# Kernel optimization log

Hardware: AMD Instinct MI355X
Metric: run time of the kernel (lower is better)

The kernel has to match this reference:

```python
import jax, jax.numpy as jnp
import numpy as np

COMMITMENT_COST = 0.25
LAMBDA_KL = 1.0
EPS = 1e-10


def setup_inputs() -> dict:
    key = jax.random.key(0)
    k1, k2 = jax.random.split(key)
    x = jax.random.normal(k1, (8, 4096, 256), dtype=jnp.float32)
    embedding = jax.random.normal(k2, (1024, 256), dtype=jnp.float32)
    return {"x": x, "embedding": embedding}


def reference(x, embedding):
    B, T, D = x.shape
    M, _ = embedding.shape
    x_sg = jax.lax.stop_gradient(x)
    x_flat = x_sg.reshape(-1, D)  # [N, D]
    distances = (jnp.sum(embedding ** 2, axis=1)[None, :]
                 + jnp.sum(x_flat ** 2, axis=1, keepdims=True)
                 - 2.0 * (x_flat @ embedding.T))  # [N, M]
    indices = jnp.argmin(distances.astype(jnp.float32), axis=-1)  # [N]
    quantized = embedding[indices].reshape(B, T, D)
    # losses (x detached in both terms, matching torch)
    loss = (COMMITMENT_COST * jnp.mean((x_sg - quantized) ** 2)
            + jnp.mean((quantized - x_sg) ** 2)) * LAMBDA_KL
    # straight-through estimator
    quantized_st = x + jax.lax.stop_gradient(quantized - x)
    # avg of one-hot encodings == normalized code counts (avoids NxM one-hot)
    N = B * T
    counts = jnp.zeros((M,), dtype=jnp.float32).at[indices].add(1.0)
    avg_probs = counts / N
    perplexity = jnp.exp(-jnp.sum(avg_probs * jnp.log(avg_probs + EPS)))
    return (quantized_st, loss, indices.reshape(B, T), perplexity)
```

## Files before the change

### kernel.cpp

```cpp
#include <hip/hip_runtime.h>


constexpr int D = 256;
constexpr int M = 1024;
constexpr int ROWS = 64;

typedef _Float16 f16;
typedef __attribute__((ext_vector_type(8))) _Float16 f16x8;
typedef __attribute__((ext_vector_type(4))) float f32x4;

constexpr size_t WS_ENORM_F = 1028;
constexpr size_t WS_TAB_B   = 8320;
constexpr size_t WS_NEEDED  = 1056896;

__device__ inline void gload_lds16(const void* g, void* l) {
    __builtin_amdgcn_global_load_lds(
        (const __attribute__((address_space(1))) unsigned int*)(g),
        (__attribute__((address_space(3))) unsigned int*)(l), 16, 0, 0);
}

__global__ __launch_bounds__(256) void prep_kernel(const float* __restrict__ e,
                                                   float* __restrict__ ws) {
    const int b = blockIdx.x, t = threadIdx.x;
    if (b < 256) {
        int v    = b * 256 + t;
        int lane = v & 63, unit = v >> 6;
        int spl = unit & 1, kk = (unit >> 1) & 7, t16 = unit >> 4;
        int lr = lane & 15, q = lane >> 4;
        const float* p = e + (size_t)(t16 * 16 + lr) * D + kk * 32 + q * 8;
        f32x4 a = *reinterpret_cast<const f32x4*>(p);
        f32x4 c = *reinterpret_cast<const f32x4*>(p + 4);
        f16 h0=(f16)a.x,h1=(f16)a.y,h2=(f16)a.z,h3=(f16)a.w;
        f16 h4=(f16)c.x,h5=(f16)c.y,h6=(f16)c.z,h7=(f16)c.w;
        f16x8 out;
        if (spl == 0) out = (f16x8){h0,h1,h2,h3,h4,h5,h6,h7};
        else          out = (f16x8){(f16)(a.x-(float)h0),(f16)(a.y-(float)h1),
                                    (f16)(a.z-(float)h2),(f16)(a.w-(float)h3),
                                    (f16)(c.x-(float)h4),(f16)(c.y-(float)h5),
                                    (f16)(c.z-(float)h6),(f16)(c.w-(float)h7)};
        *reinterpret_cast<f16x8*>((char*)ws + WS_TAB_B + (size_t)v * 16) = out;
    } else {
        int row  = (b - 256) * 4 + (t >> 6);
        int lane = t & 63;
        f32x4 a = *reinterpret_cast<const f32x4*>(e + (size_t)row * D + lane * 4);
        float s = fmaf(a.x, a.x, fmaf(a.y, a.y, fmaf(a.z, a.z, a.w * a.w)));
#pragma unroll
        for (int o = 32; o > 0; o >>= 1) s += __shfl_down(s, o, 64);
        if (lane == 0) ws[WS_ENORM_F + row] = s;
    }
}

__global__ __launch_bounds__(256, 2) void vq_fused_kernel(
    const float* __restrict__ x, const float* __restrict__ e,
    float* __restrict__ outQ, float* __restrict__ outIdx, float* __restrict__ ws)
{
    __shared__ ushort ebuf[2][2][8192];
    __shared__ float  en_s[M];
    __shared__ float  wval[4][32];
    __shared__ int    widx[4][32];
    __shared__ float  xns[ROWS];
    __shared__ int    fidx[ROWS];

    const int tid   = threadIdx.x;
    const int w     = __builtin_amdgcn_readfirstlane(tid >> 6);
    const int l     = tid & 63;
    const int lr    = l & 15, q = l >> 4;
    const int rpair = w >> 1;
    const int mhalf = w & 1;
    const int R     = blockIdx.x * ROWS;
    const char* tab = (const char*)ws + WS_TAB_B;

    auto stage = [&](int buf, int g) {
#pragma unroll
        for (int i = 0; i < 8; ++i) {
            int S = w * 8 + i, half = S >> 4, sg = S & 15;
            gload_lds16(tab + (size_t)(g + half * 32) * 16384 + sg * 1024 + l * 16,
                        &ebuf[buf][half][sg * 512]);
        }
    };
    stage(0, 0);

    {
        f32x4 v = *reinterpret_cast<const f32x4*>(ws + WS_ENORM_F + tid * 4);
        *reinterpret_cast<f32x4*>(&en_s[tid * 4]) = v;
    }

    f16x8 Xh[2][8], Xl[2][8];
    float xn[2];
#pragma unroll
    for (int cf = 0; cf < 2; ++cf) {
        float s = 0.f;
#pragma unroll
        for (int kk = 0; kk < 8; ++kk) {
            const float* p = x + (size_t)(R + rpair * 32 + cf * 16 + lr) * D + kk * 32 + q * 8;
            f32x4 a = *reinterpret_cast<const f32x4*>(p);
            f32x4 c = *reinterpret_cast<const f32x4*>(p + 4);
            f16 h0=(f16)a.x,h1=(f16)a.y,h2=(f16)a.z,h3=(f16)a.w;
            f16 h4=(f16)c.x,h5=(f16)c.y,h6=(f16)c.z,h7=(f16)c.w;
            Xh[cf][kk] = (f16x8){h0,h1,h2,h3,h4,h5,h6,h7};
            Xl[cf][kk] = (f16x8){(f16)(a.x-(float)h0),(f16)(a.y-(float)h1),
                                 (f16)(a.z-(float)h2),(f16)(a.w-(float)h3),
                                 (f16)(c.x-(float)h4),(f16)(c.y-(float)h5),
                                 (f16)(c.z-(float)h6),(f16)(c.w-(float)h7)};
            s = fmaf(a.x,a.x,fmaf(a.y,a.y,fmaf(a.z,a.z,fmaf(a.w,a.w,
                fmaf(c.x,c.x,fmaf(c.y,c.y,fmaf(c.z,c.z,fmaf(c.w,c.w,s))))))));
        }
        s += __shfl_xor(s, 16, 64);
        s += __shfl_xor(s, 32, 64);
        xn[cf] = s;
    }
    __syncthreads();

    float bV[2] = {3.4e38f, 3.4e38f};
    int   bI[2] = {0, 0};

    for (int g = 0; g < 32; ++g) {
        const ushort* eb = &ebuf[g & 1][mhalf][0];
        if (g < 31) stage((g + 1) & 1, g + 1);

        f32x4 accA0 = (f32x4){0.f,0.f,0.f,0.f};
        f32x4 accB0 = (f32x4){0.f,0.f,0.f,0.f};
        f32x4 accA1 = (f32x4){0.f,0.f,0.f,0.f};
        f32x4 accB1 = (f32x4){0.f,0.f,0.f,0.f};
        __builtin_amdgcn_s_setprio(1);
#pragma unroll
        for (int kk = 0; kk < 8; ++kk) {
            f16x8 Ah = *reinterpret_cast<const f16x8*>(eb + (kk*2+0)*512 + l*8);
            f16x8 Al = *reinterpret_cast<const f16x8*>(eb + (kk*2+1)*512 + l*8);
            accA0 = __builtin_amdgcn_mfma_f32_16x16x32_f16(Ah, Xh[0][kk], accA0, 0, 0, 0);
            accA1 = __builtin_amdgcn_mfma_f32_16x16x32_f16(Ah, Xh[1][kk], accA1, 0, 0, 0);
            accB0 = __builtin_amdgcn_mfma_f32_16x16x32_f16(Al, Xh[0][kk], accB0, 0, 0, 0);
            accB1 = __builtin_amdgcn_mfma_f32_16x16x32_f16(Al, Xh[1][kk], accB1, 0, 0, 0);
            accA0 = __builtin_amdgcn_mfma_f32_16x16x32_f16(Ah, Xl[0][kk], accA0, 0, 0, 0);
            accA1 = __builtin_amdgcn_mfma_f32_16x16x32_f16(Ah, Xl[1][kk], accA1, 0, 0, 0);
        }
        __builtin_amdgcn_s_setprio(0);
        __syncthreads();

        const int mbase = mhalf * 512 + g * 16;
        f32x4 en4 = *reinterpret_cast<const f32x4*>(&en_s[mbase + q * 4]);
#pragma unroll
        for (int i = 0; i < 4; ++i) {
            int mi = mbase + q * 4 + i;
            float dv0 = fmaf(-2.f, accA0[i] + accB0[i], en4[i]);
            float dv1 = fmaf(-2.f, accA1[i] + accB1[i], en4[i]);
            if (dv0 < bV[0]) { bV[0] = dv0; bI[0] = mi; }
            if (dv1 < bV[1]) { bV[1] = dv1; bI[1] = mi; }
        }
    }

#pragma unroll
    for (int cf = 0; cf < 2; ++cf) {
#pragma unroll
        for (int mk = 16; mk <= 32; mk <<= 1) {
            float ov = __shfl_xor(bV[cf], mk, 64);
            int   oi = __shfl_xor(bI[cf], mk, 64);
            if (ov < bV[cf] || (ov == bV[cf] && oi < bI[cf])) { bV[cf] = ov; bI[cf] = oi; }
        }
    }
    if (q == 0) {
#pragma unroll
        for (int cf = 0; cf < 2; ++cf) {
            wval[w][cf * 16 + lr] = bV[cf];
            widx[w][cf * 16 + lr] = bI[cf];
        }
        if (mhalf == 0) {
#pragma unroll
            for (int cf = 0; cf < 2; ++cf)
                xns[rpair * 32 + cf * 16 + lr] = xn[cf];
        }
    }
    __syncthreads();

    if (tid < 64) {
        int r = tid, g2 = r >> 5, rr = r & 31;
        float v0 = wval[g2 * 2 + 0][rr]; int i0 = widx[g2 * 2 + 0][rr];
        float v1 = wval[g2 * 2 + 1][rr]; int i1 = widx[g2 * 2 + 1][rr];
        float fv; int fi;
        if (v1 < v0) { fv = v1; fi = i1; } else { fv = v0; fi = i0; }
        fidx[r] = fi;
        outIdx[R + r] = (float)fi;
        atomicAdd(ws + 1 + fi, 1.0f);
        float ls = fv + xns[r];
#pragma unroll
        for (int o = 32; o > 0; o >>= 1) ls += __shfl_down(ls, o, 64);
        if (r == 0) atomicAdd(ws, ls);
    }
    __syncthreads();

#pragma unroll
    for (int it = 0; it < 16; ++it) {
        int u = it * 256 + tid;
        int row = u >> 6, c4 = u & 63;
        f32x4 v = *reinterpret_cast<const f32x4*>(e + (size_t)fidx[row] * D + c4 * 4);
        __builtin_nontemporal_store(v, reinterpret_cast<f32x4*>(outQ + (size_t)(R + row) * D + c4 * 4));
    }
}

__global__ void enorm_kernel(const float* __restrict__ e, float* __restrict__ enorm) {
    int m = blockIdx.x, l = threadIdx.x;
    const f32x4 v = *reinterpret_cast<const f32x4*>(e + m * D + l * 4);
    float s = fmaf(v.x, v.x, fmaf(v.y, v.y, fmaf(v.z, v.z, v.w * v.w)));
#pragma unroll
    for (int o = 32; o > 0; o >>= 1) s += __shfl_down(s, o, 64);
    if (l == 0) enorm[m] = s;
}

__global__ __launch_bounds__(256, 2) void vq_main_kernel(
    const float* __restrict__ x, const float* __restrict__ e,
    float* __restrict__ outQ, float* __restrict__ outIdx, float* __restrict__ ws) {
    __shared__ f32x4 xs[64][64];
    __shared__ float cval[4][64];
    __shared__ int   cidx[4][64];
    __shared__ int   fidx[64];
    const int tid = threadIdx.x, row0 = blockIdx.x * 64;
#pragma unroll
    for (int it = 0; it < 16; ++it) {
        int f = it * 256 + tid, rr = f >> 6, c4 = f & 63;
        xs[rr][c4 ^ (rr & 7)] = *reinterpret_cast<const f32x4*>(x + (row0 + rr) * D + c4 * 4);
    }
    __syncthreads();
    const int r = tid & 63, c = __builtin_amdgcn_readfirstlane(tid >> 6), sw = r & 7;
    float xnorm = 0.f;
    if (c == 0) {
        f32x4 a = (f32x4){0.f,0.f,0.f,0.f};
        for (int d4 = 0; d4 < 64; ++d4) {
            f32x4 xv = xs[r][d4 ^ sw];
            a.x = fmaf(xv.x, xv.x, a.x); a.y = fmaf(xv.y, xv.y, a.y);
            a.z = fmaf(xv.z, xv.z, a.z); a.w = fmaf(xv.w, xv.w, a.w);
        }
        xnorm = (a.x + a.y) + (a.z + a.w);
    }
    const float* __restrict__ enorm = ws + WS_ENORM_F;
    float bestVal = 3.4e38f; int bestIdx = 0;
    for (int chunk = 0; chunk < M / 32; ++chunk) {
        const int m0 = chunk * 32 + c * 8;
        f32x4 acc[8];
#pragma unroll
        for (int mi = 0; mi < 8; ++mi) acc[mi] = (f32x4){0.f,0.f,0.f,0.f};
#pragma unroll 2
        for (int d4 = 0; d4 < 64; ++d4) {
            const f32x4 xv = xs[r][d4 ^ sw];
#pragma unroll
            for (int mi = 0; mi < 8; ++mi) {
                const f32x4 ev = *reinterpret_cast<const f32x4*>(e + (m0 + mi) * D + d4 * 4);
                acc[mi].x = fmaf(xv.x, ev.x, acc[mi].x); acc[mi].y = fmaf(xv.y, ev.y, acc[mi].y);
                acc[mi].z = fmaf(xv.z, ev.z, acc[mi].z); acc[mi].w = fmaf(xv.w, ev.w, acc[mi].w);
            }
        }
#pragma unroll
        for (int mi = 0; mi < 8; ++mi) {
            float dot = (acc[mi].x + acc[mi].y) + (acc[mi].z + acc[mi].w);
            float val = enorm[m0 + mi] - 2.0f * dot;
            if (val < bestVal) { bestVal = val; bestIdx = m0 + mi; }
        }
    }
    cval[c][r] = bestVal; cidx[c][r] = bestIdx;
    __syncthreads();
    if (c == 0) {
        float bv = bestVal; int bi = bestIdx;
#pragma unroll
        for (int cc = 1; cc < 4; ++cc) {
            float v = cval[cc][r]; int i = cidx[cc][r];
            if (v < bv || (v == bv && i < bi)) { bv = v; bi = i; }
        }
        fidx[r] = bi; outIdx[row0 + r] = (float)bi;
        atomicAdd(ws + 1 + bi, 1.0f);
        float dist = bv + xnorm;
#pragma unroll
        for (int o = 32; o > 0; o >>= 1) dist += __shfl_down(dist, o, 64);
        if (r == 0) atomicAdd(ws, dist);
    }
    __syncthreads();
#pragma unroll
    for (int it = 0; it < 16; ++it) {
        int f = it * 256 + tid, rr = f >> 6, c4 = f & 63;
        *reinterpret_cast<f32x4*>(outQ + (row0 + rr) * D + c4 * 4) =
            *reinterpret_cast<const f32x4*>(e + fidx[rr] * D + c4 * 4);
    }
}

__global__ void vq_final_kernel(const float* __restrict__ ws,
                                float* __restrict__ outLoss, float* __restrict__ outPpl,
                                float invN, float invND) {
    int t = threadIdx.x;
    float p = ws[1 + t] * invN;
    float term = p * logf(p + 1e-10f);
#pragma unroll
    for (int o = 32; o > 0; o >>= 1) term += __shfl_down(term, o, 64);
    __shared__ float s[16];
    if ((t & 63) == 0) s[t >> 6] = term;
    __syncthreads();
    if (t == 0) {
        float tot = 0.f;
#pragma unroll
        for (int i = 0; i < 16; ++i) tot += s[i];
        *outPpl  = expf(-tot);
        *outLoss = 1.25f * ws[0] * invND;
    }
}

extern "C" void kernel_launch(void* const* d_in, const int* in_sizes, int n_in,
                              void* d_out, int out_size, void* d_ws, size_t ws_size,
                              hipStream_t stream) {
    const float* x = (const float*)d_in[0];
    const float* e = (const float*)d_in[1];
    const int NX = in_sizes[0];
    const int N  = NX / D;

    float* out     = (float*)d_out;
    float* outQ    = out;
    float* outLoss = out + NX;
    float* outIdx  = out + NX + 1;
    float* outPpl  = out + NX + 1 + N;
    float* ws      = (float*)d_ws;

    (void)hipMemsetAsync(d_ws, 0, 4100, stream);
    if (ws_size >= WS_NEEDED && (N % ROWS) == 0) {
        prep_kernel<<<512, 256, 0, stream>>>(e, ws);
        vq_fused_kernel<<<N / ROWS, 256, 0, stream>>>(x, e, outQ, outIdx, ws);
    } else {
        enorm_kernel<<<M, 64, 0, stream>>>(e, ws + WS_ENORM_F);
        vq_main_kernel<<<N / 64, 256, 0, stream>>>(x, e, outQ, outIdx, ws);
    }
    vq_final_kernel<<<1, 1024, 0, stream>>>(ws, outLoss, outPpl,
                                            1.0f / (float)N, 1.0f / (float)NX);
}
```

Before: 86.48 us.

## Switch distance GEMM to 32x32x16 MFMA with re-laid-out codebook table

Replaces the 16x16x32 MFMA tiling with 32x32x16 MFMAs, so each wave handles 32 rows against 32 codes per tile and the k dimension is split across two staged buffers per tile. The prep kernel writes the f16 hi/lo codebook table in a matching layout, and the argmin epilogue is reworked for the new accumulator layout. The workspace memset is folded into an extra prep block to drop a separate memset launch. The larger MFMA shape is meant to raise matrix-core throughput and cut instruction count, at the cost of more VGPRs for X fragments and more syncs per tile.

```diff
diff --git a/kernel.cpp b/kernel.cpp
--- a/kernel.cpp
+++ b/kernel.cpp
@@ -6,8 +6,9 @@
 constexpr int ROWS = 64;
 
 typedef _Float16 f16;
-typedef __attribute__((ext_vector_type(8))) _Float16 f16x8;
-typedef __attribute__((ext_vector_type(4))) float f32x4;
+typedef __attribute__((ext_vector_type(8)))  _Float16 f16x8;
+typedef __attribute__((ext_vector_type(4)))  float f32x4;
+typedef __attribute__((ext_vector_type(16))) float f32x16;
 
 constexpr size_t WS_ENORM_F = 1028;
 constexpr size_t WS_TAB_B   = 8320;
@@ -24,10 +25,12 @@
     const int b = blockIdx.x, t = threadIdx.x;
     if (b < 256) {
         int v    = b * 256 + t;
-        int lane = v & 63, unit = v >> 6;
-        int spl = unit & 1, kk = (unit >> 1) & 7, t16 = unit >> 4;
-        int lr = lane & 15, q = lane >> 4;
-        const float* p = e + (size_t)(t16 * 16 + lr) * D + kk * 32 + q * 8;
+        int lane = v & 63, u = (v >> 6) & 15;
+        int ksl  = (v >> 10) & 1, t32 = v >> 11;
+        int kstep = u & 7, spl = u >> 3;
+        int row  = t32 * 32 + (lane & 31);
+        int col0 = (ksl * 8 + kstep) * 16 + (lane >> 5) * 8;
+        const float* p = e + (size_t)row * D + col0;
         f32x4 a = *reinterpret_cast<const f32x4*>(p);
         f32x4 c = *reinterpret_cast<const f32x4*>(p + 4);
         f16 h0=(f16)a.x,h1=(f16)a.y,h2=(f16)a.z,h3=(f16)a.w;
@@ -39,7 +42,7 @@
                                     (f16)(c.x-(float)h4),(f16)(c.y-(float)h5),
                                     (f16)(c.z-(float)h6),(f16)(c.w-(float)h7)};
         *reinterpret_cast<f16x8*>((char*)ws + WS_TAB_B + (size_t)v * 16) = out;
-    } else {
+    } else if (b < 512) {
         int row  = (b - 256) * 4 + (t >> 6);
         int lane = t & 63;
         f32x4 a = *reinterpret_cast<const f32x4*>(e + (size_t)row * D + lane * 4);
@@ -47,6 +50,8 @@
 #pragma unroll
         for (int o = 32; o > 0; o >>= 1) s += __shfl_down(s, o, 64);
         if (lane == 0) ws[WS_ENORM_F + row] = s;
+    } else {
+        for (int i = t; i < 1026; i += 256) ws[i] = 0.f;
     }
 }
 
@@ -64,17 +69,19 @@
     const int tid   = threadIdx.x;
     const int w     = __builtin_amdgcn_readfirstlane(tid >> 6);
     const int l     = tid & 63;
-    const int lr    = l & 15, q = l >> 4;
     const int rpair = w >> 1;
     const int mhalf = w & 1;
     const int R     = blockIdx.x * ROWS;
+    const int xr    = l & 31;
+    const int kg    = l >> 5;
     const char* tab = (const char*)ws + WS_TAB_B;
 
     auto stage = [&](int buf, int g) {
+        int tt = g >> 1, ks = g & 1;
 #pragma unroll
         for (int i = 0; i < 8; ++i) {
             int S = w * 8 + i, half = S >> 4, sg = S & 15;
-            gload_lds16(tab + (size_t)(g + half * 32) * 16384 + sg * 1024 + l * 16,
+            gload_lds16(tab + (size_t)(((half * 16 + tt) * 2 + ks)) * 16384 + sg * 1024 + l * 16,
                         &ebuf[buf][half][sg * 512]);
         }
     };
@@ -85,90 +92,87 @@
         *reinterpret_cast<f32x4*>(&en_s[tid * 4]) = v;
     }
 
-    f16x8 Xh[2][8], Xl[2][8];
-    float xn[2];
-#pragma unroll
-    for (int cf = 0; cf < 2; ++cf) {
+    f16x8 Xh[16], Xl[16];
+    float xn;
+    {
         float s = 0.f;
 #pragma unroll
-        for (int kk = 0; kk < 8; ++kk) {
-            const float* p = x + (size_t)(R + rpair * 32 + cf * 16 + lr) * D + kk * 32 + q * 8;
+        for (int ku = 0; ku < 16; ++ku) {
+            const float* p = x + (size_t)(R + rpair * 32 + xr) * D + ku * 16 + kg * 8;
             f32x4 a = *reinterpret_cast<const f32x4*>(p);
             f32x4 c = *reinterpret_cast<const f32x4*>(p + 4);
             f16 h0=(f16)a.x,h1=(f16)a.y,h2=(f16)a.z,h3=(f16)a.w;
             f16 h4=(f16)c.x,h5=(f16)c.y,h6=(f16)c.z,h7=(f16)c.w;
-            Xh[cf][kk] = (f16x8){h0,h1,h2,h3,h4,h5,h6,h7};
-            Xl[cf][kk] = (f16x8){(f16)(a.x-(float)h0),(f16)(a.y-(float)h1),
-                                 (f16)(a.z-(float)h2),(f16)(a.w-(float)h3),
-                                 (f16)(c.x-(float)h4),(f16)(c.y-(float)h5),
-                                 (f16)(c.z-(float)h6),(f16)(c.w-(float)h7)};
+            Xh[ku] = (f16x8){h0,h1,h2,h3,h4,h5,h6,h7};
+            Xl[ku] = (f16x8){(f16)(a.x-(float)h0),(f16)(a.y-(float)h1),
+                             (f16)(a.z-(float)h2),(f16)(a.w-(float)h3),
+                             (f16)(c.x-(float)h4),(f16)(c.y-(float)h5),
+                             (f16)(c.z-(float)h6),(f16)(c.w-(float)h7)};
             s = fmaf(a.x,a.x,fmaf(a.y,a.y,fmaf(a.z,a.z,fmaf(a.w,a.w,
                 fmaf(c.x,c.x,fmaf(c.y,c.y,fmaf(c.z,c.z,fmaf(c.w,c.w,s))))))));
         }
-        s += __shfl_xor(s, 16, 64);
         s += __shfl_xor(s, 32, 64);
-        xn[cf] = s;
-    }
-    __syncthreads();
-
-    float bV[2] = {3.4e38f, 3.4e38f};
-    int   bI[2] = {0, 0};
-
-    for (int g = 0; g < 32; ++g) {
-        const ushort* eb = &ebuf[g & 1][mhalf][0];
-        if (g < 31) stage((g + 1) & 1, g + 1);
-
-        f32x4 accA0 = (f32x4){0.f,0.f,0.f,0.f};
-        f32x4 accB0 = (f32x4){0.f,0.f,0.f,0.f};
-        f32x4 accA1 = (f32x4){0.f,0.f,0.f,0.f};
-        f32x4 accB1 = (f32x4){0.f,0.f,0.f,0.f};
+        xn = s;
+    }
+    __syncthreads();
+
+    float bV = 3.4e38f;
+    int   bI = 0;
+    const ushort* eb0 = &ebuf[0][mhalf][0];
+    const ushort* eb1 = &ebuf[1][mhalf][0];
+
+    for (int t = 0; t < 16; ++t) {
+        f32x16 accA = {0.f}, accB = {0.f};
+
+        stage(1, 2 * t + 1);
         __builtin_amdgcn_s_setprio(1);
 #pragma unroll
-        for (int kk = 0; kk < 8; ++kk) {
-            f16x8 Ah = *reinterpret_cast<const f16x8*>(eb + (kk*2+0)*512 + l*8);
-            f16x8 Al = *reinterpret_cast<const f16x8*>(eb + (kk*2+1)*512 + l*8);
-            accA0 = __builtin_amdgcn_mfma_f32_16x16x32_f16(Ah, Xh[0][kk], accA0, 0, 0, 0);
-            accA1 = __builtin_amdgcn_mfma_f32_16x16x32_f16(Ah, Xh[1][kk], accA1, 0, 0, 0);
-            accB0 = __builtin_amdgcn_mfma_f32_16x16x32_f16(Al, Xh[0][kk], accB0, 0, 0, 0);
-            accB1 = __builtin_amdgcn_mfma_f32_16x16x32_f16(Al, Xh[1][kk], accB1, 0, 0, 0);
-            accA0 = __builtin_amdgcn_mfma_f32_16x16x32_f16(Ah, Xl[0][kk], accA0, 0, 0, 0);
-            accA1 = __builtin_amdgcn_mfma_f32_16x16x32_f16(Ah, Xl[1][kk], accA1, 0, 0, 0);
+        for (int kstep = 0; kstep < 8; ++kstep) {
+            f16x8 Ah = *reinterpret_cast<const f16x8*>(eb0 + kstep * 512 + l * 8);
+            f16x8 Al = *reinterpret_cast<const f16x8*>(eb0 + (8 + kstep) * 512 + l * 8);
+            accA = __builtin_amdgcn_mfma_f32_32x32x16_f16(Ah, Xh[kstep], accA, 0, 0, 0);
+            accB = __builtin_amdgcn_mfma_f32_32x32x16_f16(Al, Xh[kstep], accB, 0, 0, 0);
+            accA = __builtin_amdgcn_mfma_f32_32x32x16_f16(Ah, Xl[kstep], accA, 0, 0, 0);
         }
         __builtin_amdgcn_s_setprio(0);
         __syncthreads();
 
-        const int mbase = mhalf * 512 + g * 16;
-        f32x4 en4 = *reinterpret_cast<const f32x4*>(&en_s[mbase + q * 4]);
-#pragma unroll
-        for (int i = 0; i < 4; ++i) {
-            int mi = mbase + q * 4 + i;
-            float dv0 = fmaf(-2.f, accA0[i] + accB0[i], en4[i]);
-            float dv1 = fmaf(-2.f, accA1[i] + accB1[i], en4[i]);
-            if (dv0 < bV[0]) { bV[0] = dv0; bI[0] = mi; }
-            if (dv1 < bV[1]) { bV[1] = dv1; bI[1] = mi; }
-        }
-    }
-
-#pragma unroll
-    for (int cf = 0; cf < 2; ++cf) {
-#pragma unroll
-        for (int mk = 16; mk <= 32; mk <<= 1) {
-            float ov = __shfl_xor(bV[cf], mk, 64);
-            int   oi = __shfl_xor(bI[cf], mk, 64);
-            if (ov < bV[cf] || (ov == bV[cf] && oi < bI[cf])) { bV[cf] = ov; bI[cf] = oi; }
-        }
-    }
-    if (q == 0) {
-#pragma unroll
-        for (int cf = 0; cf < 2; ++cf) {
-            wval[w][cf * 16 + lr] = bV[cf];
-            widx[w][cf * 16 + lr] = bI[cf];
-        }
-        if (mhalf == 0) {
-#pragma unroll
-            for (int cf = 0; cf < 2; ++cf)
-                xns[rpair * 32 + cf * 16 + lr] = xn[cf];
-        }
+        if (t < 15) stage(0, 2 * t + 2);
+        __builtin_amdgcn_s_setprio(1);
+#pragma unroll
+        for (int kstep = 0; kstep < 8; ++kstep) {
+            f16x8 Ah = *reinterpret_cast<const f16x8*>(eb1 + kstep * 512 + l * 8);
+            f16x8 Al = *reinterpret_cast<const f16x8*>(eb1 + (8 + kstep) * 512 + l * 8);
+            accA = __builtin_amdgcn_mfma_f32_32x32x16_f16(Ah, Xh[8 + kstep], accA, 0, 0, 0);
+            accB = __builtin_amdgcn_mfma_f32_32x32x16_f16(Al, Xh[8 + kstep], accB, 0, 0, 0);
+            accA = __builtin_amdgcn_mfma_f32_32x32x16_f16(Ah, Xl[8 + kstep], accA, 0, 0, 0);
+        }
+        __builtin_amdgcn_s_setprio(0);
+        __syncthreads();
+
+        const int mbase = mhalf * 512 + t * 32;
+#pragma unroll
+        for (int rq = 0; rq < 4; ++rq) {
+            f32x4 en4 = *reinterpret_cast<const f32x4*>(&en_s[mbase + rq * 8 + kg * 4]);
+#pragma unroll
+            for (int j = 0; j < 4; ++j) {
+                int reg = rq * 4 + j;
+                int mi  = mbase + rq * 8 + kg * 4 + j;
+                float dv = fmaf(-2.f, accA[reg] + accB[reg], en4[j]);
+                if (dv < bV) { bV = dv; bI = mi; }
+            }
+        }
+    }
+
+    {
+        float ov = __shfl_xor(bV, 32, 64);
+        int   oi = __shfl_xor(bI, 32, 64);
+        if (ov < bV || (ov == bV && oi < bI)) { bV = ov; bI = oi; }
+    }
+    if (l < 32) {
+        wval[w][xr] = bV;
+        widx[w][xr] = bI;
+        if (mhalf == 0) xns[rpair * 32 + xr] = xn;
     }
     __syncthreads();
 
@@ -315,11 +319,11 @@
     float* outPpl  = out + NX + 1 + N;
     float* ws      = (float*)d_ws;
 
-    (void)hipMemsetAsync(d_ws, 0, 4100, stream);
     if (ws_size >= WS_NEEDED && (N % ROWS) == 0) {
-        prep_kernel<<<512, 256, 0, stream>>>(e, ws);
+        prep_kernel<<<513, 256, 0, stream>>>(e, ws);
         vq_fused_kernel<<<N / ROWS, 256, 0, stream>>>(x, e, outQ, outIdx, ws);
     } else {
+        (void)hipMemsetAsync(d_ws, 0, 4100, stream);
         enorm_kernel<<<M, 64, 0, stream>>>(e, ws + WS_ENORM_F);
         vq_main_kernel<<<N / 64, 256, 0, stream>>>(x, e, outQ, outIdx, ws);
     }
```

Result: faster. 80.22 us (-7.2%).
